# Performance work log

Measured on AMD Instinct MI355X. Metric: run time of the kernel, lower is better.

The kernel has to match this reference:

```python
import jax, jax.numpy as jnp
import numpy as np

ZONEOUT = 0.1
OUT_CHANNELS = 80
REDUCTION_FACTOR = 2


def setup_inputs() -> dict:
    key = jax.random.key(0)
    ks = jax.random.split(key, 7)
    B, H, T, L = 64, 1024, 500, 2
    s = 1.0 / np.sqrt(H)
    return {
        "res_output": jax.random.normal(ks[0], (B, H, T), dtype=jnp.float32),
        "Wih": jax.random.normal(ks[1], (L, 3 * H, H), dtype=jnp.float32) * s,
        "Whh": jax.random.normal(ks[2], (L, 3 * H, H), dtype=jnp.float32) * s,
        "bih": jax.random.normal(ks[3], (L, 3 * H), dtype=jnp.float32) * s,
        "bhh": jax.random.normal(ks[4], (L, 3 * H), dtype=jnp.float32) * s,
        "Wout": jax.random.normal(ks[5], (OUT_CHANNELS * 2, H), dtype=jnp.float32) * s,
        "bout": jax.random.normal(ks[6], (OUT_CHANNELS * 2,), dtype=jnp.float32) * s,
    }


def _gru_cell(x, h, wih, whh, bi, bh):
    # torch.nn.GRUCell math
    gi = x @ wih.T + bi            # (B, 3H)
    gh = h @ whh.T + bh            # (B, 3H)
    i_r, i_z, i_n = jnp.split(gi, 3, axis=-1)
    h_r, h_z, h_n = jnp.split(gh, 3, axis=-1)
    r = jax.nn.sigmoid(i_r + h_r)
    z = jax.nn.sigmoid(i_z + h_z)
    n = jnp.tanh(i_n + r * h_n)
    return (1.0 - z) * n + z * h


def reference(res_output, Wih, Whh, bih, bhh, Wout, bout):
    B, H, T = res_output.shape
    L = Wih.shape[0]
    xs = jnp.transpose(res_output, (2, 0, 1))  # (T, B, H)

    def step(hs, x):
        new_hs = []
        inp = x
        for l in range(L):  # static small layer loop
            h_new = _gru_cell(inp, hs[l], Wih[l], Whh[l], bih[l], bhh[l])
            # eval-mode zoneout: deterministic blend
            h_new = ZONEOUT * hs[l] + (1.0 - ZONEOUT) * h_new
            new_hs.append(h_new)
            inp = h_new
        y = inp @ Wout.T + bout  # (B, 2*out_channels)
        return tuple(new_hs), y

    h0 = tuple(jnp.zeros((B, H), dtype=res_output.dtype) for _ in range(L))
    _, ys = jax.lax.scan(step, h0, xs)  # (T, B, 2*oc)
    ys = ys.reshape(T, B, OUT_CHANNELS, REDUCTION_FACTOR)
    # concat per-step (B, oc, rf) blocks along last dim -> (B, oc, T*rf)
    out = jnp.transpose(ys, (1, 2, 0, 3)).reshape(B, OUT_CHANNELS, T * REDUCTION_FACTOR)
    return out
```

## Files before the change

kernel.cpp:

```cpp
#include <hip/hip_runtime.h>

typedef __attribute__((ext_vector_type(8))) short bhalf8;
typedef __attribute__((ext_vector_type(4))) float floatx4;

#define NSLOTS 502
#define NWG 64
#define BLOCK 768

#define AS1 __attribute__((address_space(1)))
#define AS3 __attribute__((address_space(3)))
#define GLL_COH(g, s)   __builtin_amdgcn_global_load_lds((const AS1 unsigned*)(g), (AS3 unsigned*)(s), 16, 0, 17)
#define GLL_PLAIN(g, s) __builtin_amdgcn_global_load_lds((const AS1 unsigned*)(g), (AS3 unsigned*)(s), 16, 0, 0)

__device__ __forceinline__ unsigned short f2b(float f) {
  unsigned u = __float_as_uint(f);
  return (unsigned short)((u + 0x7FFFu + ((u >> 16) & 1u)) >> 16);
}

__device__ __forceinline__ unsigned long long cload(const unsigned long long* p) {
  return __hip_atomic_load(p, __ATOMIC_RELAXED, __HIP_MEMORY_SCOPE_AGENT);
}
__device__ __forceinline__ void cstore(unsigned long long* p, unsigned long long v) {
  __hip_atomic_store(p, v, __ATOMIC_RELAXED, __HIP_MEMORY_SCOPE_AGENT);
}

__global__ void prep_w(const float* __restrict__ wih, const float* __restrict__ whh,
                       const float* __restrict__ wout,
                       unsigned short* __restrict__ wihb, unsigned short* __restrict__ whhb,
                       unsigned short* __restrict__ woutb) {
  size_t i0 = (size_t)blockIdx.x * blockDim.x + threadIdx.x;
  size_t stride = (size_t)gridDim.x * blockDim.x;
  for (size_t i = i0; i < 6291456u; i += stride) { wihb[i] = f2b(wih[i]); whhb[i] = f2b(whh[i]); }
  for (size_t i = i0; i < 163840u; i += stride) woutb[i] = f2b(wout[i]);
}

__global__ void prep_x(const float* __restrict__ x, unsigned short* __restrict__ xb) {
  __shared__ float tile[32][33];
  int b = blockIdx.z;
  int h0 = blockIdx.y * 32, t0 = blockIdx.x * 32;
  int tx = threadIdx.x, ty = threadIdx.y;
  #pragma unroll
  for (int i = 0; i < 32; i += 8) {
    int t = t0 + tx;
    if (t < 500) tile[ty + i][tx] = x[((size_t)b * 1024 + h0 + ty + i) * 500 + t];
  }
  __syncthreads();
  #pragma unroll
  for (int i = 0; i < 32; i += 8) {
    int t = t0 + ty + i;
    if (t < 500) xb[((size_t)t * 64 + b) * 1024 + h0 + tx] = f2b(tile[tx][ty + i]);
  }
}


__launch_bounds__(BLOCK, 1)
__global__ void gru_main(const unsigned short* __restrict__ xb,
                         const unsigned short* __restrict__ wihb,
                         const unsigned short* __restrict__ whhb,
                         const unsigned short* __restrict__ woutb,
                         const float* __restrict__ bih, const float* __restrict__ bhh,
                         const float* __restrict__ bout,
                         char* __restrict__ wsb, float* __restrict__ out) {
  int* cnt = (int*)wsb;
  int* rel = (int*)(wsb + 2048);
  char* h0b[2] = { wsb + 4096, wsb + 135168 };
  char* h1b[2] = { wsb + 266240, wsb + 397312 };

  const int wg = blockIdx.x;
  const int layer = wg >> 5;
  const int c = wg & 31;
  const int n0 = c * 32;
  const int tid = threadIdx.x;
  const int w = tid >> 6;
  const int l = tid & 63;
  const int l15 = l & 15, l4 = l >> 4;
  const int sd = w / 6;
  const int rr6 = w % 6;
  const int g = rr6 >> 1;
  const int u = rr6 & 1;

  __shared__ __align__(16) char smem[131072];

  const unsigned short* Wside = (sd == 0 ? wihb : whhb) + (size_t)layer * 3145728;
  const unsigned short* wbase = Wside + (size_t)(g * 1024 + n0 + u * 16 + l15) * 1024 + l4 * 8;
  bhalf8 wreg[32];
  #pragma unroll
  for (int kl = 0; kl < 32; ++kl) wreg[kl] = *(const bhalf8*)(wbase + kl * 32);

  const float* bi = bih + layer * 3072;
  const float* bh = bhh + layer * 3072;
  float bir[3][4], bhr[3][4];
  {
    int j0 = (tid & 7) << 2;
    #pragma unroll
    for (int q = 0; q < 4; ++q) {
      int n = n0 + j0 + q;
      #pragma unroll
      for (int gg = 0; gg < 3; ++gg) { bir[gg][q] = bi[gg * 1024 + n]; bhr[gg][q] = bh[gg * 1024 + n]; }
    }
  }
  float hcr[4] = {0.f, 0.f, 0.f, 0.f};

  int dead = 0;

  for (int s = 0; s < NSLOTS; ++s) {
    const int p = s & 1;
    const bool activeL = (layer == 0) ? (s <= 499) : (s >= 1 && s <= 500);

    if (activeL) {
      const char* src0;
      const char* src1;
      char* houtb;
      if (layer == 0) {
        src0 = (const char*)xb + (size_t)s * 131072;
        src1 = h0b[p ^ 1];
        houtb = h0b[p];
      } else {
        src0 = h0b[p ^ 1];
        src1 = h1b[p];
        houtb = h1b[p ^ 1];
      }
      const bool s0plain = (layer == 0);

      auto issue_chunk = [&](int kc) {
        if (w < 8) {
          const char* sb = (w < 4) ? src0 : src1;
          char* bufb = smem + ((kc & 3) << 15) + ((w >> 2) << 14);
          #pragma unroll
          for (int i = 0; i < 4; ++i) {
            int q = ((w & 3) << 2) + i;
            int row = (q << 2) + l4;
            int colb = l15 << 4;
            const char* ga = sb + row * 2048 + kc * 256 + (colb ^ ((row & 7) << 4));
            char* la = bufb + (q << 10);
            if (s0plain && w < 4) GLL_PLAIN(ga, la); else GLL_COH(ga, la);
          }
        }
      };

      floatx4 acc[4];
      #pragma unroll
      for (int m = 0; m < 4; ++m) acc[m] = (floatx4){0.f, 0.f, 0.f, 0.f};

      issue_chunk(0); issue_chunk(1); issue_chunk(2);

      #pragma unroll
      for (int kc = 0; kc < 8; ++kc) {
        if (kc <= 5)      asm volatile("s_waitcnt vmcnt(8)" ::: "memory");
        else if (kc == 6) asm volatile("s_waitcnt vmcnt(4)" ::: "memory");
        else              asm volatile("s_waitcnt vmcnt(0)" ::: "memory");
        __builtin_amdgcn_s_barrier();
        __builtin_amdgcn_sched_barrier(0);
        const char* Ab = smem + ((kc & 3) << 15) + (sd << 14);
        #pragma unroll
        for (int klL = 0; klL < 4; ++klL) {
          #pragma unroll
          for (int m = 0; m < 4; ++m) {
            int row = m * 16 + l15;
            bhalf8 a = *(const bhalf8*)(Ab + row * 256 + ((klL * 64 + l4 * 16) ^ ((row & 7) << 4)));
            acc[m] = __builtin_amdgcn_mfma_f32_16x16x32_bf16(a, wreg[kc * 4 + klL], acc[m], 0, 0, 0);
          }
        }
        if (kc < 5) issue_chunk(kc + 3);
        __builtin_amdgcn_sched_barrier(0);
      }
      __syncthreads();

      float* Gsf = (float*)smem;
      int pl = (sd * 3 + g) * 2176;
      #pragma unroll
      for (int m = 0; m < 4; ++m)
        #pragma unroll
        for (int i = 0; i < 4; ++i)
          Gsf[pl + (m * 16 + l4 * 4 + i) * 34 + u * 16 + l15] = acc[m][i];
      __syncthreads();

      if (tid < 512) {
        int b = tid >> 3, j0 = (tid & 7) << 2;
        union { unsigned long long ull; unsigned short us[4]; } pk;
        #pragma unroll
        for (int q = 0; q < 4; ++q) {
          int j = j0 + q;
          float ir  = Gsf[0 * 2176 + b * 34 + j] + bir[0][q];
          float iz  = Gsf[1 * 2176 + b * 34 + j] + bir[1][q];
          float inn = Gsf[2 * 2176 + b * 34 + j] + bir[2][q];
          float hr  = Gsf[3 * 2176 + b * 34 + j] + bhr[0][q];
          float hz  = Gsf[4 * 2176 + b * 34 + j] + bhr[1][q];
          float hn  = Gsf[5 * 2176 + b * 34 + j] + bhr[2][q];
          float rg = 1.f / (1.f + expf(-(ir + hr)));
          float zg = 1.f / (1.f + expf(-(iz + hz)));
          float nc = tanhf(inn + rg * hn);
          float hp = hcr[q];
          float hnew = (1.f - zg) * nc + zg * hp;
          float hzo = 0.1f * hp + 0.9f * hnew;
          hcr[q] = hzo;
          pk.us[q] = f2b(hzo);
        }
        cstore((unsigned long long*)(houtb + (size_t)b * 2048 + ((n0 + j0) << 1)), pk.ull);
      }
    }

    if (s < NSLOTS - 1) {
      __syncthreads();
      if (tid == 0) {
        int old = __hip_atomic_fetch_add(&cnt[s], 1, __ATOMIC_RELAXED, __HIP_MEMORY_SCOPE_AGENT);
        if (old == NWG - 1)
          __hip_atomic_store(&rel[s], 1, __ATOMIC_RELAXED, __HIP_MEMORY_SCOPE_AGENT);
      }
      if (layer == 0 && c < 20 && s >= 2 && w < 2) {
        int tau = c * 2 + w;
        int bt = tau / 10, ct = tau % 10;
        const char* Ay = h1b[p];
        const unsigned long long* arow =
            (const unsigned long long*)(Ay + (size_t)(bt * 16 + l15) * 2048);
        const unsigned short* brow = woutb + (size_t)(ct * 16 + l15) * 1024;
        floatx4 accy = (floatx4){0.f, 0.f, 0.f, 0.f};
        #pragma unroll
        for (int ks = 0; ks < 32; ++ks) {
          int kg = ks * 32 + l4 * 8;
          union { unsigned long long uu[2]; bhalf8 v; } av;
          av.uu[0] = cload(arow + (kg >> 2));
          av.uu[1] = cload(arow + (kg >> 2) + 1);
          bhalf8 bb = *(const bhalf8*)(brow + kg);
          accy = __builtin_amdgcn_mfma_f32_16x16x32_bf16(av.v, bb, accy, 0, 0, 0);
        }
        int col = ct * 16 + l15;
        float bo = bout[col];
        int t2 = s - 2;
        #pragma unroll
        for (int i = 0; i < 4; ++i) {
          int b = bt * 16 + l4 * 4 + i;
          out[(size_t)b * 80000 + (size_t)(col >> 1) * 1000 + t2 * 2 + (col & 1)] = accy[i] + bo;
        }
      }
      __syncthreads();
      if (tid == 0 && !dead) {
        int it = 0;
        while (__hip_atomic_load(&rel[s], __ATOMIC_RELAXED, __HIP_MEMORY_SCOPE_AGENT) == 0) {
          __builtin_amdgcn_s_sleep(2);
          if (++it > 1000000) { dead = 1; break; }
        }
      }
      __syncthreads();
    } else {
      if (layer == 0 && c < 20 && w < 2) {
        int tau = c * 2 + w;
        int bt = tau / 10, ct = tau % 10;
        const char* Ay = h1b[p];
        const unsigned long long* arow =
            (const unsigned long long*)(Ay + (size_t)(bt * 16 + l15) * 2048);
        const unsigned short* brow = woutb + (size_t)(ct * 16 + l15) * 1024;
        floatx4 accy = (floatx4){0.f, 0.f, 0.f, 0.f};
        #pragma unroll
        for (int ks = 0; ks < 32; ++ks) {
          int kg = ks * 32 + l4 * 8;
          union { unsigned long long uu[2]; bhalf8 v; } av;
          av.uu[0] = cload(arow + (kg >> 2));
          av.uu[1] = cload(arow + (kg >> 2) + 1);
          bhalf8 bb = *(const bhalf8*)(brow + kg);
          accy = __builtin_amdgcn_mfma_f32_16x16x32_bf16(av.v, bb, accy, 0, 0, 0);
        }
        int col = ct * 16 + l15;
        float bo = bout[col];
        int t2 = s - 2;
        #pragma unroll
        for (int i = 0; i < 4; ++i) {
          int b = bt * 16 + l4 * 4 + i;
          out[(size_t)b * 80000 + (size_t)(col >> 1) * 1000 + t2 * 2 + (col & 1)] = accy[i] + bo;
        }
      }
    }
  }
}

extern "C" void kernel_launch(void* const* d_in, const int* in_sizes, int n_in,
                              void* d_out, int out_size, void* d_ws, size_t ws_size,
                              hipStream_t stream) {
  const float* res  = (const float*)d_in[0];
  const float* Wih  = (const float*)d_in[1];
  const float* Whh  = (const float*)d_in[2];
  const float* bih  = (const float*)d_in[3];
  const float* bhh  = (const float*)d_in[4];
  const float* Wout = (const float*)d_in[5];
  const float* bout = (const float*)d_in[6];
  float* out = (float*)d_out;
  char* ws = (char*)d_ws;
  if (ws_size < 91557888u) return;

  unsigned short* woutb = (unsigned short*)(ws + 528384);
  unsigned short* wihb  = (unsigned short*)(ws + 856064);
  unsigned short* whhb  = (unsigned short*)(ws + 13438976);
  unsigned short* xb    = (unsigned short*)(ws + 26021888);

  hipMemsetAsync(ws, 0, 528384, stream);
  prep_w<<<4096, 256, 0, stream>>>(Wih, Whh, Wout, wihb, whhb, woutb);
  prep_x<<<dim3(16, 32, 64), dim3(32, 8), 0, stream>>>(res, xb);
  gru_main<<<NWG, BLOCK, 0, stream>>>(xb, wihb, whhb, woutb, bih, bhh, bout, ws, out);
}
```

Measured before the change: 14.07 ms.

## Replace global barrier with per-workgroup flags and split layer-1 across batch halves

Replaces the all-workgroup counter/release barrier per slot with per-workgroup progress flags, so each workgroup waits only on the producers it actually depends on. Layer 0 gets a triple-buffered h0 so it can run ahead of layer 1. Layer 1 is spread over 64 workgroups, each handling half the batch, and the output projection moves into layer-1 workgroups, reading h1 from LDS instead of coherent global loads. The x prefetch for the next slot is issued before the dependency wait to hide latency. The cost is more workgroups, more LDS, and a subtler dependency protocol that could race if the flag thresholds are wrong.

```diff
diff --git a/kernel.cpp b/kernel.cpp
--- a/kernel.cpp
+++ b/kernel.cpp
@@ -4,7 +4,7 @@
 typedef __attribute__((ext_vector_type(4))) float floatx4;
 
 #define NSLOTS 502
-#define NWG 64
+#define NWG 96
 #define BLOCK 768
 
 #define AS1 __attribute__((address_space(1)))
@@ -16,12 +16,11 @@
   unsigned u = __float_as_uint(f);
   return (unsigned short)((u + 0x7FFFu + ((u >> 16) & 1u)) >> 16);
 }
-
-__device__ __forceinline__ unsigned long long cload(const unsigned long long* p) {
-  return __hip_atomic_load(p, __ATOMIC_RELAXED, __HIP_MEMORY_SCOPE_AGENT);
-}
 __device__ __forceinline__ void cstore(unsigned long long* p, unsigned long long v) {
   __hip_atomic_store(p, v, __ATOMIC_RELAXED, __HIP_MEMORY_SCOPE_AGENT);
+}
+__device__ __forceinline__ int cloadi(const int* p) {
+  return __hip_atomic_load(p, __ATOMIC_RELAXED, __HIP_MEMORY_SCOPE_AGENT);
 }
 
 __global__ void prep_w(const float* __restrict__ wih, const float* __restrict__ whh,
@@ -61,31 +60,31 @@
                          const float* __restrict__ bih, const float* __restrict__ bhh,
                          const float* __restrict__ bout,
                          char* __restrict__ wsb, float* __restrict__ out) {
-  int* cnt = (int*)wsb;
-  int* rel = (int*)(wsb + 2048);
-  char* h0b[2] = { wsb + 4096, wsb + 135168 };
-  char* h1b[2] = { wsb + 266240, wsb + 397312 };
+  int* flg = (int*)wsb;
+  char* h0b[3] = { wsb + 1024, wsb + 132096, wsb + 263168 };
+  char* h1b[2] = { wsb + 394240, wsb + 525312 };
 
   const int wg = blockIdx.x;
-  const int layer = wg >> 5;
-  const int c = wg & 31;
+  const int layer = (wg < 32) ? 0 : 1;
+  const int idx1 = wg - 32;
+  const int c    = (layer == 0) ? wg : (idx1 & 31);
+  const int half = (layer == 0) ? 0  : (idx1 >> 5);
   const int n0 = c * 32;
   const int tid = threadIdx.x;
   const int w = tid >> 6;
   const int l = tid & 63;
   const int l15 = l & 15, l4 = l >> 4;
   const int sd = w / 6;
-  const int rr6 = w % 6;
-  const int g = rr6 >> 1;
-  const int u = rr6 & 1;
-
-  __shared__ __align__(16) char smem[131072];
+  const int g = (w % 6) >> 1;
+  const int u = w & 1;
+
+  __shared__ __align__(16) char smem[155648];
 
   const unsigned short* Wside = (sd == 0 ? wihb : whhb) + (size_t)layer * 3145728;
   const unsigned short* wbase = Wside + (size_t)(g * 1024 + n0 + u * 16 + l15) * 1024 + l4 * 8;
   bhalf8 wreg[32];
   #pragma unroll
-  for (int kl = 0; kl < 32; ++kl) wreg[kl] = *(const bhalf8*)(wbase + kl * 32);
+  for (int kk = 0; kk < 32; ++kk) wreg[kk] = *(const bhalf8*)(wbase + kk * 32);
 
   const float* bi = bih + layer * 3072;
   const float* bh = bhh + layer * 3072;
@@ -104,68 +103,100 @@
   int dead = 0;
 
   for (int s = 0; s < NSLOTS; ++s) {
-    const int p = s & 1;
-    const bool activeL = (layer == 0) ? (s <= 499) : (s >= 1 && s <= 500);
-
-    if (activeL) {
-      const char* src0;
-      const char* src1;
-      char* houtb;
-      if (layer == 0) {
-        src0 = (const char*)xb + (size_t)s * 131072;
-        src1 = h0b[p ^ 1];
-        houtb = h0b[p];
-      } else {
-        src0 = h0b[p ^ 1];
-        src1 = h1b[p];
-        houtb = h1b[p ^ 1];
-      }
-      const bool s0plain = (layer == 0);
-
-      auto issue_chunk = [&](int kc) {
-        if (w < 8) {
-          const char* sb = (w < 4) ? src0 : src1;
-          char* bufb = smem + ((kc & 3) << 15) + ((w >> 2) << 14);
+    #pragma unroll
+    for (int i = 0; i < 32; ++i) asm volatile("" : "+v"(wreg[i]));
+
+    const char* xsrc = (const char*)xb + (size_t)s * 131072;
+    const bool actL0 = (layer == 0) && (s <= 499);
+    const bool actL1 = (layer == 1) && (s >= 1 && s <= 500);
+
+    if (actL0 && w >= 8) {
+      #pragma unroll
+      for (int kcp = 0; kcp < 2; ++kcp) {
+        #pragma unroll
+        for (int i = 0; i < 2; ++i) {
+          int idx = (w - 8) * 2 + i;
+          int row = idx * 8 + (l >> 3);
+          const char* ga = xsrc + row * 2048 + kcp * 128 + (((l & 7) * 16) ^ ((row & 7) << 4));
+          GLL_PLAIN(ga, smem + 131072 + kcp * 8192 + idx * 1024);
+        }
+      }
+      __builtin_amdgcn_sched_barrier(0);
+    }
+
+    if (s > 0) {
+      if (w == 0 && !dead) {
+        int it = 0;
+        for (;;) {
+          int f = cloadi(&flg[l]);
+          int f2 = (l < 32) ? cloadi(&flg[64 + l]) : 0x7fffffff;
+          int ok;
+          if (layer == 0)
+            ok = (f >= (l < 32 ? s : s - 1)) && (f2 >= s - 1);
+          else
+            ok = (f >= s) && (f2 >= s);
+          if (__all(ok)) break;
+          __builtin_amdgcn_s_sleep(2);
+          if (++it > 2000000) { dead = 1; break; }
+        }
+      }
+      __builtin_amdgcn_s_barrier();
+      __builtin_amdgcn_sched_barrier(0);
+    }
+
+    if (actL0) {
+      const char* h0src = h0b[(s + 2) % 3];
+      char* hout = h0b[s % 3];
+      if (w < 8) {
+        #pragma unroll
+        for (int i = 0; i < 16; ++i) {
+          int idx = w + i * 8;
+          int row = idx >> 1;
+          int colb = (idx & 1) * 1024 + l * 16;
+          GLL_COH(h0src + row * 2048 + (colb ^ ((row & 7) << 4)), smem + idx * 1024);
+        }
+      }
+      asm volatile("s_waitcnt vmcnt(0)" ::: "memory");
+      __builtin_amdgcn_s_barrier();
+      __builtin_amdgcn_sched_barrier(0);
+
+      floatx4 acc[4];
+      #pragma unroll
+      for (int m = 0; m < 4; ++m) acc[m] = (floatx4){0.f, 0.f, 0.f, 0.f};
+
+      #pragma unroll
+      for (int kc = 0; kc < 16; ++kc) {
+        if (w >= 8 && kc + 2 < 16) {
+          int kc2 = kc + 2;
           #pragma unroll
-          for (int i = 0; i < 4; ++i) {
-            int q = ((w & 3) << 2) + i;
-            int row = (q << 2) + l4;
-            int colb = l15 << 4;
-            const char* ga = sb + row * 2048 + kc * 256 + (colb ^ ((row & 7) << 4));
-            char* la = bufb + (q << 10);
-            if (s0plain && w < 4) GLL_PLAIN(ga, la); else GLL_COH(ga, la);
+          for (int i = 0; i < 2; ++i) {
+            int idx = (w - 8) * 2 + i;
+            int row = idx * 8 + (l >> 3);
+            const char* ga = xsrc + row * 2048 + kc2 * 128 + (((l & 7) * 16) ^ ((row & 7) << 4));
+            GLL_PLAIN(ga, smem + 131072 + (kc2 % 3) * 8192 + idx * 1024);
           }
-        }
-      };
-
-      floatx4 acc[4];
-      #pragma unroll
-      for (int m = 0; m < 4; ++m) acc[m] = (floatx4){0.f, 0.f, 0.f, 0.f};
-
-      issue_chunk(0); issue_chunk(1); issue_chunk(2);
-
-      #pragma unroll
-      for (int kc = 0; kc < 8; ++kc) {
-        if (kc <= 5)      asm volatile("s_waitcnt vmcnt(8)" ::: "memory");
-        else if (kc == 6) asm volatile("s_waitcnt vmcnt(4)" ::: "memory");
-        else              asm volatile("s_waitcnt vmcnt(0)" ::: "memory");
-        __builtin_amdgcn_s_barrier();
-        __builtin_amdgcn_sched_barrier(0);
-        const char* Ab = smem + ((kc & 3) << 15) + (sd << 14);
-        #pragma unroll
-        for (int klL = 0; klL < 4; ++klL) {
+          __builtin_amdgcn_sched_barrier(0);
+        }
+        #pragma unroll
+        for (int klL = 0; klL < 2; ++klL) {
           #pragma unroll
           for (int m = 0; m < 4; ++m) {
             int row = m * 16 + l15;
-            bhalf8 a = *(const bhalf8*)(Ab + row * 256 + ((klL * 64 + l4 * 16) ^ ((row & 7) << 4)));
-            acc[m] = __builtin_amdgcn_mfma_f32_16x16x32_bf16(a, wreg[kc * 4 + klL], acc[m], 0, 0, 0);
+            const char* ap = (sd == 0)
+              ? smem + 131072 + (kc % 3) * 8192 + row * 128 + ((klL * 64 + l4 * 16) ^ ((row & 7) << 4))
+              : smem + row * 2048 + ((kc * 128 + klL * 64 + l4 * 16) ^ ((row & 7) << 4));
+            bhalf8 a = *(const bhalf8*)ap;
+            acc[m] = __builtin_amdgcn_mfma_f32_16x16x32_bf16(a, wreg[kc * 2 + klL], acc[m], 0, 0, 0);
           }
         }
-        if (kc < 5) issue_chunk(kc + 3);
+        if (w >= 8) {
+          if (kc <= 13)      asm volatile("s_waitcnt vmcnt(2)" ::: "memory");
+          else if (kc == 14) asm volatile("s_waitcnt vmcnt(0)" ::: "memory");
+        }
+        __builtin_amdgcn_s_barrier();
         __builtin_amdgcn_sched_barrier(0);
       }
       __syncthreads();
-
       float* Gsf = (float*)smem;
       int pl = (sd * 3 + g) * 2176;
       #pragma unroll
@@ -174,7 +205,6 @@
         for (int i = 0; i < 4; ++i)
           Gsf[pl + (m * 16 + l4 * 4 + i) * 34 + u * 16 + l15] = acc[m][i];
       __syncthreads();
-
       if (tid < 512) {
         int b = tid >> 3, j0 = (tid & 7) << 2;
         union { unsigned long long ull; unsigned short us[4]; } pk;
@@ -196,80 +226,137 @@
           hcr[q] = hzo;
           pk.us[q] = f2b(hzo);
         }
-        cstore((unsigned long long*)(houtb + (size_t)b * 2048 + ((n0 + j0) << 1)), pk.ull);
+        cstore((unsigned long long*)(hout + (size_t)b * 2048 + ((n0 + j0) << 1)), pk.ull);
+      }
+    } else if (actL1) {
+      const char* h0src = h0b[(s + 2) % 3] + (size_t)half * 32 * 2048;
+      const char* h1src = h1b[s & 1] + (size_t)half * 32 * 2048;
+      char* hout = h1b[(s & 1) ^ 1];
+      if (w < 8) {
+        #pragma unroll
+        for (int i = 0; i < 8; ++i) {
+          int idx = w + i * 8;
+          int row = idx >> 1;
+          int colb = (idx & 1) * 1024 + l * 16;
+          GLL_COH(h0src + row * 2048 + (colb ^ ((row & 7) << 4)), smem + idx * 1024);
+        }
+        #pragma unroll
+        for (int i = 0; i < 8; ++i) {
+          int idx = w + i * 8;
+          int row = idx >> 1;
+          int colb = (idx & 1) * 1024 + l * 16;
+          GLL_COH(h1src + row * 2048 + (colb ^ ((row & 7) << 4)), smem + 65536 + idx * 1024);
+        }
+      }
+      asm volatile("s_waitcnt vmcnt(0)" ::: "memory");
+      __builtin_amdgcn_s_barrier();
+      __builtin_amdgcn_sched_barrier(0);
+
+      floatx4 acc[2];
+      acc[0] = (floatx4){0.f, 0.f, 0.f, 0.f};
+      acc[1] = (floatx4){0.f, 0.f, 0.f, 0.f};
+      #pragma unroll
+      for (int kc = 0; kc < 16; ++kc)
+        #pragma unroll
+        for (int klL = 0; klL < 2; ++klL)
+          #pragma unroll
+          for (int m = 0; m < 2; ++m) {
+            int row = m * 16 + l15;
+            const char* ap = smem + sd * 65536 + row * 2048 +
+                             ((kc * 128 + klL * 64 + l4 * 16) ^ ((row & 7) << 4));
+            bhalf8 a = *(const bhalf8*)ap;
+            acc[m] = __builtin_amdgcn_mfma_f32_16x16x32_bf16(a, wreg[kc * 2 + klL], acc[m], 0, 0, 0);
+          }
+
+      if (c < 10 && w < 2 && s >= 2) {
+        const unsigned short* woutrow = woutb + (size_t)(c * 16 + l15) * 1024 + l4 * 8;
+        floatx4 accy = (floatx4){0.f, 0.f, 0.f, 0.f};
+        #pragma unroll
+        for (int kk = 0; kk < 32; ++kk) {
+          int row = w * 16 + l15;
+          const char* ap = smem + 65536 + row * 2048 + ((kk * 64 + l4 * 16) ^ ((row & 7) << 4));
+          bhalf8 a = *(const bhalf8*)ap;
+          bhalf8 bb = *(const bhalf8*)(woutrow + kk * 32);
+          accy = __builtin_amdgcn_mfma_f32_16x16x32_bf16(a, bb, accy, 0, 0, 0);
+        }
+        int col = c * 16 + l15, t2 = s - 2;
+        float bo = bout[col];
+        #pragma unroll
+        for (int i = 0; i < 4; ++i) {
+          int brow = half * 32 + w * 16 + l4 * 4 + i;
+          out[(size_t)brow * 80000 + (size_t)(col >> 1) * 1000 + t2 * 2 + (col & 1)] = accy[i] + bo;
+        }
+      }
+      __syncthreads();
+      float* Gsf = (float*)smem;
+      int pl = (sd * 3 + g) * 1088;
+      #pragma unroll
+      for (int m = 0; m < 2; ++m)
+        #pragma unroll
+        for (int i = 0; i < 4; ++i)
+          Gsf[pl + (m * 16 + l4 * 4 + i) * 34 + u * 16 + l15] = acc[m][i];
+      __syncthreads();
+      if (tid < 256) {
+        int lr = tid >> 3, j0 = (tid & 7) << 2;
+        union { unsigned long long ull; unsigned short us[4]; } pk;
+        #pragma unroll
+        for (int q = 0; q < 4; ++q) {
+          int j = j0 + q;
+          float ir  = Gsf[0 * 1088 + lr * 34 + j] + bir[0][q];
+          float iz  = Gsf[1 * 1088 + lr * 34 + j] + bir[1][q];
+          float inn = Gsf[2 * 1088 + lr * 34 + j] + bir[2][q];
+          float hr  = Gsf[3 * 1088 + lr * 34 + j] + bhr[0][q];
+          float hz  = Gsf[4 * 1088 + lr * 34 + j] + bhr[1][q];
+          float hn  = Gsf[5 * 1088 + lr * 34 + j] + bhr[2][q];
+          float rg = 1.f / (1.f + expf(-(ir + hr)));
+          float zg = 1.f / (1.f + expf(-(iz + hz)));
+          float nc = tanhf(inn + rg * hn);
+          float hp = hcr[q];
+          float hnew = (1.f - zg) * nc + zg * hp;
+          float hzo = 0.1f * hp + 0.9f * hnew;
+          hcr[q] = hzo;
+          pk.us[q] = f2b(hzo);
+        }
+        cstore((unsigned long long*)(hout + (size_t)(half * 32 + lr) * 2048 + ((n0 + j0) << 1)), pk.ull);
+      }
+    } else if (layer == 1 && s == 501) {
+      const char* h1src = h1b[s & 1] + (size_t)half * 32 * 2048;
+      if (w < 8) {
+        #pragma unroll
+        for (int i = 0; i < 8; ++i) {
+          int idx = w + i * 8;
+          int row = idx >> 1;
+          int colb = (idx & 1) * 1024 + l * 16;
+          GLL_COH(h1src + row * 2048 + (colb ^ ((row & 7) << 4)), smem + 65536 + idx * 1024);
+        }
+      }
+      asm volatile("s_waitcnt vmcnt(0)" ::: "memory");
+      __builtin_amdgcn_s_barrier();
+      __builtin_amdgcn_sched_barrier(0);
+      if (c < 10 && w < 2) {
+        const unsigned short* woutrow = woutb + (size_t)(c * 16 + l15) * 1024 + l4 * 8;
+        floatx4 accy = (floatx4){0.f, 0.f, 0.f, 0.f};
+        #pragma unroll
+        for (int kk = 0; kk < 32; ++kk) {
+          int row = w * 16 + l15;
+          const char* ap = smem + 65536 + row * 2048 + ((kk * 64 + l4 * 16) ^ ((row & 7) << 4));
+          bhalf8 a = *(const bhalf8*)ap;
+          bhalf8 bb = *(const bhalf8*)(woutrow + kk * 32);
+          accy = __builtin_amdgcn_mfma_f32_16x16x32_bf16(a, bb, accy, 0, 0, 0);
+        }
+        int col = c * 16 + l15, t2 = s - 2;
+        float bo = bout[col];
+        #pragma unroll
+        for (int i = 0; i < 4; ++i) {
+          int brow = half * 32 + w * 16 + l4 * 4 + i;
+          out[(size_t)brow * 80000 + (size_t)(col >> 1) * 1000 + t2 * 2 + (col & 1)] = accy[i] + bo;
+        }
       }
     }
 
-    if (s < NSLOTS - 1) {
-      __syncthreads();
-      if (tid == 0) {
-        int old = __hip_atomic_fetch_add(&cnt[s], 1, __ATOMIC_RELAXED, __HIP_MEMORY_SCOPE_AGENT);
-        if (old == NWG - 1)
-          __hip_atomic_store(&rel[s], 1, __ATOMIC_RELAXED, __HIP_MEMORY_SCOPE_AGENT);
-      }
-      if (layer == 0 && c < 20 && s >= 2 && w < 2) {
-        int tau = c * 2 + w;
-        int bt = tau / 10, ct = tau % 10;
-        const char* Ay = h1b[p];
-        const unsigned long long* arow =
-            (const unsigned long long*)(Ay + (size_t)(bt * 16 + l15) * 2048);
-        const unsigned short* brow = woutb + (size_t)(ct * 16 + l15) * 1024;
-        floatx4 accy = (floatx4){0.f, 0.f, 0.f, 0.f};
-        #pragma unroll
-        for (int ks = 0; ks < 32; ++ks) {
-          int kg = ks * 32 + l4 * 8;
-          union { unsigned long long uu[2]; bhalf8 v; } av;
-          av.uu[0] = cload(arow + (kg >> 2));
-          av.uu[1] = cload(arow + (kg >> 2) + 1);
-          bhalf8 bb = *(const bhalf8*)(brow + kg);
-          accy = __builtin_amdgcn_mfma_f32_16x16x32_bf16(av.v, bb, accy, 0, 0, 0);
-        }
-        int col = ct * 16 + l15;
-        float bo = bout[col];
-        int t2 = s - 2;
-        #pragma unroll
-        for (int i = 0; i < 4; ++i) {
-          int b = bt * 16 + l4 * 4 + i;
-          out[(size_t)b * 80000 + (size_t)(col >> 1) * 1000 + t2 * 2 + (col & 1)] = accy[i] + bo;
-        }
-      }
-      __syncthreads();
-      if (tid == 0 && !dead) {
-        int it = 0;
-        while (__hip_atomic_load(&rel[s], __ATOMIC_RELAXED, __HIP_MEMORY_SCOPE_AGENT) == 0) {
-          __builtin_amdgcn_s_sleep(2);
-          if (++it > 1000000) { dead = 1; break; }
-        }
-      }
-      __syncthreads();
-    } else {
-      if (layer == 0 && c < 20 && w < 2) {
-        int tau = c * 2 + w;
-        int bt = tau / 10, ct = tau % 10;
-        const char* Ay = h1b[p];
-        const unsigned long long* arow =
-            (const unsigned long long*)(Ay + (size_t)(bt * 16 + l15) * 2048);
-        const unsigned short* brow = woutb + (size_t)(ct * 16 + l15) * 1024;
-        floatx4 accy = (floatx4){0.f, 0.f, 0.f, 0.f};
-        #pragma unroll
-        for (int ks = 0; ks < 32; ++ks) {
-          int kg = ks * 32 + l4 * 8;
-          union { unsigned long long uu[2]; bhalf8 v; } av;
-          av.uu[0] = cload(arow + (kg >> 2));
-          av.uu[1] = cload(arow + (kg >> 2) + 1);
-          bhalf8 bb = *(const bhalf8*)(brow + kg);
-          accy = __builtin_amdgcn_mfma_f32_16x16x32_bf16(av.v, bb, accy, 0, 0, 0);
-        }
-        int col = ct * 16 + l15;
-        float bo = bout[col];
-        int t2 = s - 2;
-        #pragma unroll
-        for (int i = 0; i < 4; ++i) {
-          int b = bt * 16 + l4 * 4 + i;
-          out[(size_t)b * 80000 + (size_t)(col >> 1) * 1000 + t2 * 2 + (col & 1)] = accy[i] + bo;
-        }
-      }
-    }
+    __syncthreads();
+    if (tid == 0)
+      __hip_atomic_store(&flg[wg], s + 1, __ATOMIC_RELAXED, __HIP_MEMORY_SCOPE_AGENT);
   }
 }
 
@@ -285,14 +372,14 @@
   const float* bout = (const float*)d_in[6];
   float* out = (float*)d_out;
   char* ws = (char*)d_ws;
-  if (ws_size < 91557888u) return;
-
-  unsigned short* woutb = (unsigned short*)(ws + 528384);
-  unsigned short* wihb  = (unsigned short*)(ws + 856064);
-  unsigned short* whhb  = (unsigned short*)(ws + 13438976);
-  unsigned short* xb    = (unsigned short*)(ws + 26021888);
-
-  hipMemsetAsync(ws, 0, 528384, stream);
+  if (ws_size < 91685888u) return;
+
+  unsigned short* woutb = (unsigned short*)(ws + 656384);
+  unsigned short* wihb  = (unsigned short*)(ws + 984064);
+  unsigned short* whhb  = (unsigned short*)(ws + 13566976);
+  unsigned short* xb    = (unsigned short*)(ws + 26149888);
+
+  hipMemsetAsync(ws, 0, 656384, stream);
   prep_w<<<4096, 256, 0, stream>>>(Wih, Whh, Wout, wihb, whhb, woutb);
   prep_x<<<dim3(16, 32, 64), dim3(32, 8), 0, stream>>>(res, xb);
   gru_main<<<NWG, BLOCK, 0, stream>>>(xb, wihb, whhb, woutb, bih, bhh, bout, ws, out);
```

Result: slower. 26.18 ms (+86.1%).

## Replace global grid barrier with per-workgroup flags and add dedicated loader waves

Applied to the files above, without the earlier changes.

Drops the global counter/release barrier after every time slot and replaces it with per-workgroup progress flags that each workgroup polls only for the producers it depends on. Layer 0 and layer 1 can then drift apart in a pipeline, with the h0 buffer triple-buffered to make that safe. The block grows to 1024 threads so four extra waves do the global-to-LDS loads while twelve waves run MFMA. Weights are no longer held in registers and are re-read from global/L2 on every step. The output projection moves to layer-1 workgroups and converts fp32 Wout to bf16 on the fly. These trade more memory traffic per step for less synchronisation latency and better overlap.

```diff
diff --git a/kernel.cpp b/kernel.cpp
--- a/kernel.cpp
+++ b/kernel.cpp
@@ -5,7 +5,7 @@
 
 #define NSLOTS 502
 #define NWG 64
-#define BLOCK 768
+#define BLOCK 1024
 
 #define AS1 __attribute__((address_space(1)))
 #define AS3 __attribute__((address_space(3)))
@@ -16,22 +16,24 @@
   unsigned u = __float_as_uint(f);
   return (unsigned short)((u + 0x7FFFu + ((u >> 16) & 1u)) >> 16);
 }
-
-__device__ __forceinline__ unsigned long long cload(const unsigned long long* p) {
+__device__ __forceinline__ int cloadi(const int* p) {
   return __hip_atomic_load(p, __ATOMIC_RELAXED, __HIP_MEMORY_SCOPE_AGENT);
 }
-__device__ __forceinline__ void cstore(unsigned long long* p, unsigned long long v) {
+__device__ __forceinline__ void cstorei(int* p, int v) {
   __hip_atomic_store(p, v, __ATOMIC_RELAXED, __HIP_MEMORY_SCOPE_AGENT);
 }
+__device__ __forceinline__ unsigned long long cload8(const unsigned long long* p) {
+  return __hip_atomic_load(p, __ATOMIC_RELAXED, __HIP_MEMORY_SCOPE_AGENT);
+}
+__device__ __forceinline__ void cstore8(unsigned long long* p, unsigned long long v) {
+  __hip_atomic_store(p, v, __ATOMIC_RELAXED, __HIP_MEMORY_SCOPE_AGENT);
+}
 
 __global__ void prep_w(const float* __restrict__ wih, const float* __restrict__ whh,
-                       const float* __restrict__ wout,
-                       unsigned short* __restrict__ wihb, unsigned short* __restrict__ whhb,
-                       unsigned short* __restrict__ woutb) {
+                       unsigned short* __restrict__ wihb, unsigned short* __restrict__ whhb) {
   size_t i0 = (size_t)blockIdx.x * blockDim.x + threadIdx.x;
   size_t stride = (size_t)gridDim.x * blockDim.x;
   for (size_t i = i0; i < 6291456u; i += stride) { wihb[i] = f2b(wih[i]); whhb[i] = f2b(whh[i]); }
-  for (size_t i = i0; i < 163840u; i += stride) woutb[i] = f2b(wout[i]);
 }
 
 __global__ void prep_x(const float* __restrict__ x, unsigned short* __restrict__ xb) {
@@ -57,84 +59,89 @@
 __global__ void gru_main(const unsigned short* __restrict__ xb,
                          const unsigned short* __restrict__ wihb,
                          const unsigned short* __restrict__ whhb,
-                         const unsigned short* __restrict__ woutb,
+                         const float* __restrict__ wout,
                          const float* __restrict__ bih, const float* __restrict__ bhh,
                          const float* __restrict__ bout,
                          char* __restrict__ wsb, float* __restrict__ out) {
-  int* cnt = (int*)wsb;
-  int* rel = (int*)(wsb + 2048);
-  char* h0b[2] = { wsb + 4096, wsb + 135168 };
-  char* h1b[2] = { wsb + 266240, wsb + 397312 };
+  int* f0 = (int*)wsb;
+  int* f1 = (int*)(wsb + 128);
+  char* h0b = wsb + 1024;
+  char* h1b = wsb + 394240;
 
   const int wg = blockIdx.x;
   const int layer = wg >> 5;
   const int c = wg & 31;
-  const int n0 = c * 32;
+  const int n0c = c * 32;
   const int tid = threadIdx.x;
   const int w = tid >> 6;
   const int l = tid & 63;
   const int l15 = l & 15, l4 = l >> 4;
   const int sd = w / 6;
-  const int rr6 = w % 6;
-  const int g = rr6 >> 1;
-  const int u = rr6 & 1;
+  const int g = (w % 6) >> 1;
+  const int u = w & 1;
 
   __shared__ __align__(16) char smem[131072];
 
-  const unsigned short* Wside = (sd == 0 ? wihb : whhb) + (size_t)layer * 3145728;
-  const unsigned short* wbase = Wside + (size_t)(g * 1024 + n0 + u * 16 + l15) * 1024 + l4 * 8;
-  bhalf8 wreg[32];
-  #pragma unroll
-  for (int kl = 0; kl < 32; ++kl) wreg[kl] = *(const bhalf8*)(wbase + kl * 32);
-
-  const float* bi = bih + layer * 3072;
-  const float* bh = bhh + layer * 3072;
+  const unsigned short* wrow = ((sd == 0) ? wihb : whhb) + (size_t)layer * 3145728 +
+      (size_t)(g * 1024 + n0c + u * 16 + l15) * 1024 + l4 * 8;
+
   float bir[3][4], bhr[3][4];
   {
     int j0 = (tid & 7) << 2;
     #pragma unroll
-    for (int q = 0; q < 4; ++q) {
-      int n = n0 + j0 + q;
+    for (int q = 0; q < 4; ++q)
       #pragma unroll
-      for (int gg = 0; gg < 3; ++gg) { bir[gg][q] = bi[gg * 1024 + n]; bhr[gg][q] = bh[gg * 1024 + n]; }
-    }
+      for (int gg = 0; gg < 3; ++gg) {
+        bir[gg][q] = bih[layer * 3072 + gg * 1024 + n0c + j0 + q];
+        bhr[gg][q] = bhh[layer * 3072 + gg * 1024 + n0c + j0 + q];
+      }
   }
   float hcr[4] = {0.f, 0.f, 0.f, 0.f};
-
   int dead = 0;
 
   for (int s = 0; s < NSLOTS; ++s) {
-    const int p = s & 1;
-    const bool activeL = (layer == 0) ? (s <= 499) : (s >= 1 && s <= 500);
-
-    if (activeL) {
+    const bool act = (layer == 0) ? (s <= 499) : (s >= 1);
+    const bool doGemm = (layer == 0) ? (s <= 499) : (s >= 1 && s <= 500);
+
+    if (act) {
+      if (w == 0 && !dead) {
+        int it = 0;
+        for (;;) {
+          int ok;
+          if (layer == 0)
+            ok = (l < 32) ? (cloadi(&f0[l]) >= s) : (cloadi(&f1[l - 32]) >= s - 1);
+          else
+            ok = (l < 32) ? (cloadi(&f0[l]) >= s) : (cloadi(&f1[l - 32]) >= s);
+          if (__all(ok)) break;
+          __builtin_amdgcn_s_sleep(2);
+          if (++it > 300000) { dead = 1; break; }
+        }
+      }
+      __builtin_amdgcn_s_barrier();
+      __builtin_amdgcn_sched_barrier(0);
+
       const char* src0;
       const char* src1;
-      char* houtb;
       if (layer == 0) {
         src0 = (const char*)xb + (size_t)s * 131072;
-        src1 = h0b[p ^ 1];
-        houtb = h0b[p];
+        src1 = h0b + (size_t)((s + 2) % 3) * 131072;
       } else {
-        src0 = h0b[p ^ 1];
-        src1 = h1b[p];
-        houtb = h1b[p ^ 1];
-      }
-      const bool s0plain = (layer == 0);
+        src0 = h0b + (size_t)((s - 1) % 3) * 131072;
+        src1 = h1b + (size_t)(s & 1) * 131072;
+      }
 
       auto issue_chunk = [&](int kc) {
-        if (w < 8) {
-          const char* sb = (w < 4) ? src0 : src1;
-          char* bufb = smem + ((kc & 3) << 15) + ((w >> 2) << 14);
-          #pragma unroll
-          for (int i = 0; i < 4; ++i) {
-            int q = ((w & 3) << 2) + i;
-            int row = (q << 2) + l4;
-            int colb = l15 << 4;
-            const char* ga = sb + row * 2048 + kc * 256 + (colb ^ ((row & 7) << 4));
-            char* la = bufb + (q << 10);
-            if (s0plain && w < 4) GLL_PLAIN(ga, la); else GLL_COH(ga, la);
-          }
+        char* slot = smem + ((kc & 3) << 15);
+        #pragma unroll
+        for (int i = 0; i < 8; ++i) {
+          int idx = (w - 12) * 8 + i;
+          int side = idx >> 4, sub = idx & 15;
+          int row = sub * 4 + (l >> 4);
+          int kb = (l & 15) * 16;
+          const char* ga = (side ? src1 : src0) + row * 2048 + kc * 256 +
+                           (kb ^ ((row & 7) << 4));
+          char* la = slot + side * 16384 + sub * 1024;
+          if (side == 0 && layer == 0) GLL_PLAIN(ga, la); else GLL_COH(ga, la);
         }
       };
 
@@ -142,89 +149,98 @@
       #pragma unroll
       for (int m = 0; m < 4; ++m) acc[m] = (floatx4){0.f, 0.f, 0.f, 0.f};
 
-      issue_chunk(0); issue_chunk(1); issue_chunk(2);
-
-      #pragma unroll
-      for (int kc = 0; kc < 8; ++kc) {
-        if (kc <= 5)      asm volatile("s_waitcnt vmcnt(8)" ::: "memory");
-        else if (kc == 6) asm volatile("s_waitcnt vmcnt(4)" ::: "memory");
-        else              asm volatile("s_waitcnt vmcnt(0)" ::: "memory");
+      if (doGemm) {
+        if (w >= 12) {
+          issue_chunk(0); issue_chunk(1); issue_chunk(2);
+          asm volatile("s_waitcnt vmcnt(16)" ::: "memory");
+        }
         __builtin_amdgcn_s_barrier();
         __builtin_amdgcn_sched_barrier(0);
-        const char* Ab = smem + ((kc & 3) << 15) + (sd << 14);
-        #pragma unroll
-        for (int klL = 0; klL < 4; ++klL) {
+
+        #pragma unroll
+        for (int kc = 0; kc < 8; ++kc) {
+          if (w < 12) {
+            const char* Ab = smem + ((kc & 3) << 15) + sd * 16384;
+            #pragma unroll
+            for (int klL = 0; klL < 4; ++klL) {
+              bhalf8 bb = *(const bhalf8*)(wrow + (kc * 4 + klL) * 32);
+              #pragma unroll
+              for (int m = 0; m < 4; ++m) {
+                int row = m * 16 + l15;
+                bhalf8 a = *(const bhalf8*)(Ab + row * 256 +
+                           ((klL * 64 + l4 * 16) ^ ((row & 7) << 4)));
+                acc[m] = __builtin_amdgcn_mfma_f32_16x16x32_bf16(a, bb, acc[m], 0, 0, 0);
+              }
+            }
+          } else {
+            if (kc < 5) issue_chunk(kc + 3);
+            if (kc < 5)      asm volatile("s_waitcnt vmcnt(16)" ::: "memory");
+            else if (kc == 5) asm volatile("s_waitcnt vmcnt(8)" ::: "memory");
+            else if (kc == 6) asm volatile("s_waitcnt vmcnt(0)" ::: "memory");
+          }
+          __builtin_amdgcn_s_barrier();
+          __builtin_amdgcn_sched_barrier(0);
+        }
+        __syncthreads();
+
+        float* Gsf = (float*)smem;
+        if (w < 12) {
           #pragma unroll
-          for (int m = 0; m < 4; ++m) {
-            int row = m * 16 + l15;
-            bhalf8 a = *(const bhalf8*)(Ab + row * 256 + ((klL * 64 + l4 * 16) ^ ((row & 7) << 4)));
-            acc[m] = __builtin_amdgcn_mfma_f32_16x16x32_bf16(a, wreg[kc * 4 + klL], acc[m], 0, 0, 0);
+          for (int m = 0; m < 4; ++m)
+            #pragma unroll
+            for (int i = 0; i < 4; ++i)
+              Gsf[w * 1088 + (m * 16 + l4 * 4 + i) * 17 + l15] = acc[m][i];
+        }
+        __syncthreads();
+
+        if (tid < 512) {
+          int b = tid >> 3, j0 = (tid & 7) << 2;
+          char* hout = (layer == 0) ? h0b + (size_t)(s % 3) * 131072
+                                    : h1b + (size_t)((s + 1) & 1) * 131072;
+          union { unsigned long long ull; unsigned short us[4]; } pk;
+          #pragma unroll
+          for (int q = 0; q < 4; ++q) {
+            int j = j0 + q, u_ = j >> 4, jj = j & 15;
+            float gi[3], gh[3];
+            #pragma unroll
+            for (int gg = 0; gg < 3; ++gg) {
+              gi[gg] = Gsf[(0 * 6 + gg * 2 + u_) * 1088 + b * 17 + jj];
+              gh[gg] = Gsf[(1 * 6 + gg * 2 + u_) * 1088 + b * 17 + jj];
+            }
+            float ir = gi[0] + bir[0][q], iz = gi[1] + bir[1][q], inn = gi[2] + bir[2][q];
+            float hr = gh[0] + bhr[0][q], hz = gh[1] + bhr[1][q], hn = gh[2] + bhr[2][q];
+            float rg = 1.f / (1.f + expf(-(ir + hr)));
+            float zg = 1.f / (1.f + expf(-(iz + hz)));
+            float nc = tanhf(inn + rg * hn);
+            float hp = hcr[q];
+            float hnew = (1.f - zg) * nc + zg * hp;
+            float hzo = 0.1f * hp + 0.9f * hnew;
+            hcr[q] = hzo;
+            pk.us[q] = f2b(hzo);
           }
-        }
-        if (kc < 5) issue_chunk(kc + 3);
-        __builtin_amdgcn_sched_barrier(0);
-      }
-      __syncthreads();
-
-      float* Gsf = (float*)smem;
-      int pl = (sd * 3 + g) * 2176;
-      #pragma unroll
-      for (int m = 0; m < 4; ++m)
-        #pragma unroll
-        for (int i = 0; i < 4; ++i)
-          Gsf[pl + (m * 16 + l4 * 4 + i) * 34 + u * 16 + l15] = acc[m][i];
-      __syncthreads();
-
-      if (tid < 512) {
-        int b = tid >> 3, j0 = (tid & 7) << 2;
-        union { unsigned long long ull; unsigned short us[4]; } pk;
-        #pragma unroll
-        for (int q = 0; q < 4; ++q) {
-          int j = j0 + q;
-          float ir  = Gsf[0 * 2176 + b * 34 + j] + bir[0][q];
-          float iz  = Gsf[1 * 2176 + b * 34 + j] + bir[1][q];
-          float inn = Gsf[2 * 2176 + b * 34 + j] + bir[2][q];
-          float hr  = Gsf[3 * 2176 + b * 34 + j] + bhr[0][q];
-          float hz  = Gsf[4 * 2176 + b * 34 + j] + bhr[1][q];
-          float hn  = Gsf[5 * 2176 + b * 34 + j] + bhr[2][q];
-          float rg = 1.f / (1.f + expf(-(ir + hr)));
-          float zg = 1.f / (1.f + expf(-(iz + hz)));
-          float nc = tanhf(inn + rg * hn);
-          float hp = hcr[q];
-          float hnew = (1.f - zg) * nc + zg * hp;
-          float hzo = 0.1f * hp + 0.9f * hnew;
-          hcr[q] = hzo;
-          pk.us[q] = f2b(hzo);
-        }
-        cstore((unsigned long long*)(houtb + (size_t)b * 2048 + ((n0 + j0) << 1)), pk.ull);
-      }
-    }
-
-    if (s < NSLOTS - 1) {
-      __syncthreads();
-      if (tid == 0) {
-        int old = __hip_atomic_fetch_add(&cnt[s], 1, __ATOMIC_RELAXED, __HIP_MEMORY_SCOPE_AGENT);
-        if (old == NWG - 1)
-          __hip_atomic_store(&rel[s], 1, __ATOMIC_RELAXED, __HIP_MEMORY_SCOPE_AGENT);
-      }
-      if (layer == 0 && c < 20 && s >= 2 && w < 2) {
-        int tau = c * 2 + w;
-        int bt = tau / 10, ct = tau % 10;
-        const char* Ay = h1b[p];
+          cstore8((unsigned long long*)(hout + (size_t)b * 2048 + ((n0c + j0) << 1)), pk.ull);
+        }
+      }
+
+      if (layer == 1 && c < 10 && w >= 12 && s >= 2) {
+        const char* Ay = h1b + (size_t)(s & 1) * 131072;
+        int bt = w - 12;
         const unsigned long long* arow =
             (const unsigned long long*)(Ay + (size_t)(bt * 16 + l15) * 2048);
-        const unsigned short* brow = woutb + (size_t)(ct * 16 + l15) * 1024;
+        int col = c * 16 + l15;
+        const float* wr = wout + (size_t)col * 1024 + l4 * 8;
         floatx4 accy = (floatx4){0.f, 0.f, 0.f, 0.f};
         #pragma unroll
         for (int ks = 0; ks < 32; ++ks) {
           int kg = ks * 32 + l4 * 8;
           union { unsigned long long uu[2]; bhalf8 v; } av;
-          av.uu[0] = cload(arow + (kg >> 2));
-          av.uu[1] = cload(arow + (kg >> 2) + 1);
-          bhalf8 bb = *(const bhalf8*)(brow + kg);
-          accy = __builtin_amdgcn_mfma_f32_16x16x32_bf16(av.v, bb, accy, 0, 0, 0);
-        }
-        int col = ct * 16 + l15;
+          av.uu[0] = cload8(arow + (kg >> 2));
+          av.uu[1] = cload8(arow + (kg >> 2) + 1);
+          union { bhalf8 v; unsigned short us[8]; } bw;
+          #pragma unroll
+          for (int e = 0; e < 8; ++e) bw.us[e] = f2b(wr[ks * 32 + e]);
+          accy = __builtin_amdgcn_mfma_f32_16x16x32_bf16(av.v, bw.v, accy, 0, 0, 0);
+        }
         float bo = bout[col];
         int t2 = s - 2;
         #pragma unroll
@@ -233,42 +249,11 @@
           out[(size_t)b * 80000 + (size_t)(col >> 1) * 1000 + t2 * 2 + (col & 1)] = accy[i] + bo;
         }
       }
-      __syncthreads();
-      if (tid == 0 && !dead) {
-        int it = 0;
-        while (__hip_atomic_load(&rel[s], __ATOMIC_RELAXED, __HIP_MEMORY_SCOPE_AGENT) == 0) {
-          __builtin_amdgcn_s_sleep(2);
-          if (++it > 1000000) { dead = 1; break; }
-        }
-      }
-      __syncthreads();
-    } else {
-      if (layer == 0 && c < 20 && w < 2) {
-        int tau = c * 2 + w;
-        int bt = tau / 10, ct = tau % 10;
-        const char* Ay = h1b[p];
-        const unsigned long long* arow =
-            (const unsigned long long*)(Ay + (size_t)(bt * 16 + l15) * 2048);
-        const unsigned short* brow = woutb + (size_t)(ct * 16 + l15) * 1024;
-        floatx4 accy = (floatx4){0.f, 0.f, 0.f, 0.f};
-        #pragma unroll
-        for (int ks = 0; ks < 32; ++ks) {
-          int kg = ks * 32 + l4 * 8;
-          union { unsigned long long uu[2]; bhalf8 v; } av;
-          av.uu[0] = cload(arow + (kg >> 2));
-          av.uu[1] = cload(arow + (kg >> 2) + 1);
-          bhalf8 bb = *(const bhalf8*)(brow + kg);
-          accy = __builtin_amdgcn_mfma_f32_16x16x32_bf16(av.v, bb, accy, 0, 0, 0);
-        }
-        int col = ct * 16 + l15;
-        float bo = bout[col];
-        int t2 = s - 2;
-        #pragma unroll
-        for (int i = 0; i < 4; ++i) {
-          int b = bt * 16 + l4 * 4 + i;
-          out[(size_t)b * 80000 + (size_t)(col >> 1) * 1000 + t2 * 2 + (col & 1)] = accy[i] + bo;
-        }
-      }
+    }
+
+    __syncthreads();
+    if (tid == 0) {
+      if (layer == 0) cstorei(&f0[c], s + 1); else cstorei(&f1[c], s + 1);
     }
   }
 }
@@ -285,15 +270,14 @@
   const float* bout = (const float*)d_in[6];
   float* out = (float*)d_out;
   char* ws = (char*)d_ws;
-  if (ws_size < 91557888u) return;
-
-  unsigned short* woutb = (unsigned short*)(ws + 528384);
-  unsigned short* wihb  = (unsigned short*)(ws + 856064);
-  unsigned short* whhb  = (unsigned short*)(ws + 13438976);
-  unsigned short* xb    = (unsigned short*)(ws + 26021888);
-
-  hipMemsetAsync(ws, 0, 528384, stream);
-  prep_w<<<4096, 256, 0, stream>>>(Wih, Whh, Wout, wihb, whhb, woutb);
+  if (ws_size < 91358208u) return;
+
+  unsigned short* wihb = (unsigned short*)(ws + 656384);
+  unsigned short* whhb = (unsigned short*)(ws + 13239296);
+  unsigned short* xb   = (unsigned short*)(ws + 25822208);
+
+  hipMemsetAsync(ws, 0, 656384, stream);
+  prep_w<<<4096, 256, 0, stream>>>(Wih, Whh, wihb, whhb);
   prep_x<<<dim3(16, 32, 64), dim3(32, 8), 0, stream>>>(res, xb);
-  gru_main<<<NWG, BLOCK, 0, stream>>>(xb, wihb, whhb, woutb, bih, bhh, bout, ws, out);
-}
+  gru_main<<<NWG, BLOCK, 0, stream>>>(xb, wihb, whhb, Wout, bih, bhh, bout, ws, out);
+}
```

New measurement: 17.75 ms. +26.1%, slower.
